# Kernel tuning notes

Hardware: AMD Instinct MI355X
Metric: run time of the kernel (lower is better)

The kernel has to match this reference:

```python
import jax, jax.numpy as jnp
import numpy as np

LEAK_RATE = 0.1
SPIKE_THRESHOLD = 0.5
MAX_DIM = 2560
R = 2048   # reservoir dim
D = 1024   # input dim
B = 4096   # batch


def setup_inputs() -> dict:
    key = jax.random.key(0)
    k1, k2, k3, k4, k5 = jax.random.split(key, 5)
    inputs = jax.random.normal(k1, (B, D), dtype=jnp.float32)
    prev_state = jax.random.normal(k2, (B, MAX_DIM), dtype=jnp.float32)
    W_in = jax.random.normal(k3, (R, D), dtype=jnp.float32) * (1.0 / np.sqrt(D))
    W_res = jax.random.normal(k4, (R, R), dtype=jnp.float32) * (1.0 / np.sqrt(R))
    W_gate = jax.random.normal(k5, (3 * R, D), dtype=jnp.float32) * (1.0 / np.sqrt(D))
    return {"inputs": inputs, "prev_state": prev_state,
            "W_in": W_in, "W_res": W_res, "W_gate": W_gate}


def reference(inputs, prev_state, W_in, W_res, W_gate):
    # Slice state to active reservoir width (W_res.shape[0] == R)
    prev = prev_state[:, :R]                                  # [B, R]
    input_part = jnp.matmul(inputs, W_in.T)                   # [B, R]
    reservoir_part = jnp.matmul(prev, W_res.T)                # [B, R]
    gate = jax.nn.sigmoid(jnp.matmul(inputs, W_gate.T))       # [B, 3R]
    i_gate, f_gate, o_gate = jnp.split(gate, 3, axis=-1)      # each [B, R]
    state = (1.0 - LEAK_RATE) * (f_gate * prev) \
        + LEAK_RATE * jnp.tanh(i_gate * (input_part + reservoir_part))
    state = o_gate * state
    # Spike threshold + soft reset
    state = jnp.where(state > SPIKE_THRESHOLD, state - SPIKE_THRESHOLD, state)
    # Pad up to max dynamic reservoir dim
    padded = jnp.pad(state, ((0, 0), (0, MAX_DIM - R)))       # [B, MAX_DIM]
    return padded
```

## Files before the change

kernel.cpp:

```cpp
#include <hip/hip_runtime.h>

#define B_  4096
#define D_  1024
#define R_  2048
#define MAXD 2560

typedef _Float16 half8 __attribute__((ext_vector_type(8)));
typedef _Float16 half4 __attribute__((ext_vector_type(4)));
typedef float    f32x4 __attribute__((ext_vector_type(4)));

constexpr int BM = 128;
constexpr int BN = 64;
constexpr int BK = 32;
constexpr int SAS = 40;

__device__ inline float sigmoidf_(float x) { return 1.0f / (1.0f + expf(-x)); }

__global__ __launch_bounds__(256, 2)
void reservoir_fused(const float* __restrict__ X,
                     const float* __restrict__ P,
                     const float* __restrict__ Win,
                     const float* __restrict__ Wres,
                     const float* __restrict__ Wg,
                     float* __restrict__ out)
{
    __shared__ _Float16 sAh[BM * SAS];
    __shared__ _Float16 sAl[BM * SAS];
    __shared__ _Float16 sWh[4][BN * SAS];
    __shared__ _Float16 sWl[4][BN * SAS];

    const int tid  = threadIdx.x;
    const int lane = tid & 63;
    const int wv   = tid >> 6;
    const int m0   = blockIdx.y * BM;
    const int n0   = blockIdx.x * BN;

    f32x4 acc[4][2][4];
    #pragma unroll
    for (int s = 0; s < 4; ++s)
        #pragma unroll
        for (int mt = 0; mt < 2; ++mt)
            #pragma unroll
            for (int nt = 0; nt < 4; ++nt) acc[s][mt][nt] = (f32x4){0.f, 0.f, 0.f, 0.f};

    const int fr = lane & 15;
    const int fk = (lane >> 4) * 8;

    for (int k0 = 0; k0 < D_ + R_; k0 += BK) {
        const bool ph1 = (k0 < D_);

        {
            const float* src; int ld, kc;
            if (ph1) { src = X; ld = D_;   kc = k0; }
            else     { src = P; ld = MAXD; kc = k0 - D_; }
            #pragma unroll
            for (int i = 0; i < 4; ++i) {
                int f = i * 256 + tid;
                int row = f >> 3, c4 = (f & 7) * 4;
                f32x4 v = *(const f32x4*)(src + (size_t)(m0 + row) * ld + kc + c4);
                half4 h, l;
                #pragma unroll
                for (int j = 0; j < 4; ++j) {
                    h[j] = (_Float16)v[j];
                    l[j] = (_Float16)(v[j] - (float)h[j]);
                }
                *(half4*)(&sAh[row * SAS + c4]) = h;
                *(half4*)(&sAl[row * SAS + c4]) = l;
            }
        }
        {
            const float* src; int ld, kc;
            if (ph1) { src = Win;  ld = D_; kc = k0; }
            else     { src = Wres; ld = R_; kc = k0 - D_; }
            #pragma unroll
            for (int i = 0; i < 2; ++i) {
                int f = i * 256 + tid;
                int row = f >> 3, c4 = (f & 7) * 4;
                f32x4 v = *(const f32x4*)(src + (size_t)(n0 + row) * ld + kc + c4);
                half4 h, l;
                #pragma unroll
                for (int j = 0; j < 4; ++j) {
                    h[j] = (_Float16)v[j];
                    l[j] = (_Float16)(v[j] - (float)h[j]);
                }
                *(half4*)(&sWh[0][row * SAS + c4]) = h;
                *(half4*)(&sWl[0][row * SAS + c4]) = l;
            }
        }
        if (ph1) {
            #pragma unroll
            for (int g = 0; g < 3; ++g)
                #pragma unroll
                for (int i = 0; i < 2; ++i) {
                    int f = i * 256 + tid;
                    int row = f >> 3, c4 = (f & 7) * 4;
                    f32x4 v = *(const f32x4*)(Wg + (size_t)(g * R_ + n0 + row) * D_ + k0 + c4);
                    half4 h, l;
                    #pragma unroll
                    for (int j = 0; j < 4; ++j) {
                        h[j] = (_Float16)v[j];
                        l[j] = (_Float16)(v[j] - (float)h[j]);
                    }
                    *(half4*)(&sWh[1 + g][row * SAS + c4]) = h;
                    *(half4*)(&sWl[1 + g][row * SAS + c4]) = l;
                }
        }
        __syncthreads();

        half8 ah0 = *(const half8*)(&sAh[(wv * 32 +      fr) * SAS + fk]);
        half8 al0 = *(const half8*)(&sAl[(wv * 32 +      fr) * SAS + fk]);
        half8 ah1 = *(const half8*)(&sAh[(wv * 32 + 16 + fr) * SAS + fk]);
        half8 al1 = *(const half8*)(&sAl[(wv * 32 + 16 + fr) * SAS + fk]);

        const int nsets = ph1 ? 4 : 1;
        #pragma unroll
        for (int s = 0; s < 4; ++s) {
            if (s < nsets) {
                #pragma unroll
                for (int nt = 0; nt < 4; ++nt) {
                    half8 bh = *(const half8*)(&sWh[s][(nt * 16 + fr) * SAS + fk]);
                    half8 bl = *(const half8*)(&sWl[s][(nt * 16 + fr) * SAS + fk]);
                    acc[s][0][nt] = __builtin_amdgcn_mfma_f32_16x16x32_f16(ah0, bh, acc[s][0][nt], 0, 0, 0);
                    acc[s][0][nt] = __builtin_amdgcn_mfma_f32_16x16x32_f16(al0, bh, acc[s][0][nt], 0, 0, 0);
                    acc[s][0][nt] = __builtin_amdgcn_mfma_f32_16x16x32_f16(ah0, bl, acc[s][0][nt], 0, 0, 0);
                    acc[s][1][nt] = __builtin_amdgcn_mfma_f32_16x16x32_f16(ah1, bh, acc[s][1][nt], 0, 0, 0);
                    acc[s][1][nt] = __builtin_amdgcn_mfma_f32_16x16x32_f16(al1, bh, acc[s][1][nt], 0, 0, 0);
                    acc[s][1][nt] = __builtin_amdgcn_mfma_f32_16x16x32_f16(ah1, bl, acc[s][1][nt], 0, 0, 0);
                }
            }
        }
        __syncthreads();
    }

    const int qd = lane >> 4;
    #pragma unroll
    for (int mt = 0; mt < 2; ++mt)
        #pragma unroll
        for (int nt = 0; nt < 4; ++nt)
            #pragma unroll
            for (int r = 0; r < 4; ++r) {
                int row = m0 + wv * 32 + mt * 16 + qd * 4 + r;
                int col = n0 + nt * 16 + fr;
                float pre = acc[0][mt][nt][r];
                float ig  = sigmoidf_(acc[1][mt][nt][r]);
                float fg  = sigmoidf_(acc[2][mt][nt][r]);
                float og  = sigmoidf_(acc[3][mt][nt][r]);
                float pv  = P[(size_t)row * MAXD + col];
                float st  = 0.9f * (fg * pv) + 0.1f * tanhf(ig * pre);
                st *= og;
                if (st > 0.5f) st -= 0.5f;
                out[(size_t)row * MAXD + col] = st;
            }
}

__global__ void pad_zero(float* __restrict__ out) {
    int idx = blockIdx.x * 256 + threadIdx.x;
    int row = idx >> 7;
    int c   = (idx & 127) * 4;
    *(f32x4*)(&out[(size_t)row * MAXD + R_ + c]) = (f32x4){0.f, 0.f, 0.f, 0.f};
}

extern "C" void kernel_launch(void* const* d_in, const int* in_sizes, int n_in,
                              void* d_out, int out_size, void* d_ws, size_t ws_size,
                              hipStream_t stream) {
    const float* X    = (const float*)d_in[0];
    const float* P    = (const float*)d_in[1];
    const float* Win  = (const float*)d_in[2];
    const float* Wres = (const float*)d_in[3];
    const float* Wg   = (const float*)d_in[4];
    float* out        = (float*)d_out;

    pad_zero<<<2048, 256, 0, stream>>>(out);
    dim3 grid(R_ / BN, B_ / BM);
    reservoir_fused<<<grid, 256, 0, stream>>>(X, P, Win, Wres, Wg, out);
}
```

Baseline: 526.0 us.

## Switch to 32x32x16 MFMA with 2x2 wave tiling and fragment-ordered LDS layout

Replaces the 16x16x32 MFMA tiles with 32x32x16 MFMA and reorganises the four waves into a 2x2 grid, each covering 64 rows by 32 columns. Shared memory is rewritten into a fragment-major layout so each lane reads its 8-half fragment contiguously, removing the padded row stride. The aim is fewer LDS reads per MFMA, no bank conflicts, and higher MFMA throughput per instruction. The epilogue index mapping changes to the 32x32 accumulator layout, which risks correctness errors if the mapping is wrong.

```diff
diff --git a/kernel.cpp b/kernel.cpp
--- a/kernel.cpp
+++ b/kernel.cpp
@@ -5,15 +5,23 @@
 #define R_  2048
 #define MAXD 2560
 
-typedef _Float16 half8 __attribute__((ext_vector_type(8)));
-typedef _Float16 half4 __attribute__((ext_vector_type(4)));
-typedef float    f32x4 __attribute__((ext_vector_type(4)));
+typedef _Float16 half4v __attribute__((ext_vector_type(4)));
+typedef _Float16 half8v __attribute__((ext_vector_type(8)));
+typedef float    f32x4  __attribute__((ext_vector_type(4)));
+typedef float    f32x16 __attribute__((ext_vector_type(16)));
 
 constexpr int BM = 128;
 constexpr int BN = 64;
 constexpr int BK = 32;
-constexpr int SAS = 40;
 
+
+__device__ inline void split4(const f32x4 v, half4v& h, half4v& l) {
+    #pragma unroll
+    for (int j = 0; j < 4; ++j) {
+        h[j] = (_Float16)v[j];
+        l[j] = (_Float16)(v[j] - (float)h[j]);
+    }
+}
 __device__ inline float sigmoidf_(float x) { return 1.0f / (1.0f + expf(-x)); }
 
 __global__ __launch_bounds__(256, 2)
@@ -24,27 +32,24 @@
                      const float* __restrict__ Wg,
                      float* __restrict__ out)
 {
-    __shared__ _Float16 sAh[BM * SAS];
-    __shared__ _Float16 sAl[BM * SAS];
-    __shared__ _Float16 sWh[4][BN * SAS];
-    __shared__ _Float16 sWl[4][BN * SAS];
+    __shared__ _Float16 sAh[4096], sAl[4096];
+    __shared__ _Float16 sWh[4][2048], sWl[4][2048];
 
     const int tid  = threadIdx.x;
     const int lane = tid & 63;
     const int wv   = tid >> 6;
+    const int wm   = wv >> 1;
+    const int wn   = wv & 1;
     const int m0   = blockIdx.y * BM;
     const int n0   = blockIdx.x * BN;
 
-    f32x4 acc[4][2][4];
+    f32x16 acc[4][2];
     #pragma unroll
     for (int s = 0; s < 4; ++s)
         #pragma unroll
-        for (int mt = 0; mt < 2; ++mt)
+        for (int mb = 0; mb < 2; ++mb)
             #pragma unroll
-            for (int nt = 0; nt < 4; ++nt) acc[s][mt][nt] = (f32x4){0.f, 0.f, 0.f, 0.f};
-
-    const int fr = lane & 15;
-    const int fk = (lane >> 4) * 8;
+            for (int r = 0; r < 16; ++r) acc[s][mb][r] = 0.0f;
 
     for (int k0 = 0; k0 < D_ + R_; k0 += BK) {
         const bool ph1 = (k0 < D_);
@@ -55,17 +60,13 @@
             else     { src = P; ld = MAXD; kc = k0 - D_; }
             #pragma unroll
             for (int i = 0; i < 4; ++i) {
-                int f = i * 256 + tid;
-                int row = f >> 3, c4 = (f & 7) * 4;
-                f32x4 v = *(const f32x4*)(src + (size_t)(m0 + row) * ld + kc + c4);
-                half4 h, l;
-                #pragma unroll
-                for (int j = 0; j < 4; ++j) {
-                    h[j] = (_Float16)v[j];
-                    l[j] = (_Float16)(v[j] - (float)h[j]);
-                }
-                *(half4*)(&sAh[row * SAS + c4]) = h;
-                *(half4*)(&sAl[row * SAS + c4]) = l;
+                int t = i * 256 + tid;
+                int r = t >> 3, sel = t & 7, kq = sel >> 1, h4 = sel & 1;
+                f32x4 v = *(const f32x4*)(src + (size_t)(m0 + r) * ld + kc + kq * 8 + h4 * 4);
+                half4v h, l; split4(v, h, l);
+                int off = ((r >> 5) * 2 + (kq >> 1)) * 512 + ((((kq & 1) << 5) | (r & 31)) * 8) + h4 * 4;
+                *(half4v*)(&sAh[off]) = h;
+                *(half4v*)(&sAl[off]) = l;
             }
         }
         {
@@ -74,17 +75,13 @@
             else     { src = Wres; ld = R_; kc = k0 - D_; }
             #pragma unroll
             for (int i = 0; i < 2; ++i) {
-                int f = i * 256 + tid;
-                int row = f >> 3, c4 = (f & 7) * 4;
-                f32x4 v = *(const f32x4*)(src + (size_t)(n0 + row) * ld + kc + c4);
-                half4 h, l;
-                #pragma unroll
-                for (int j = 0; j < 4; ++j) {
-                    h[j] = (_Float16)v[j];
-                    l[j] = (_Float16)(v[j] - (float)h[j]);
-                }
-                *(half4*)(&sWh[0][row * SAS + c4]) = h;
-                *(half4*)(&sWl[0][row * SAS + c4]) = l;
+                int t = i * 256 + tid;
+                int r = t >> 3, sel = t & 7, kq = sel >> 1, h4 = sel & 1;
+                f32x4 v = *(const f32x4*)(src + (size_t)(n0 + r) * ld + kc + kq * 8 + h4 * 4);
+                half4v h, l; split4(v, h, l);
+                int off = ((r >> 5) * 2 + (kq >> 1)) * 512 + ((((kq & 1) << 5) | (r & 31)) * 8) + h4 * 4;
+                *(half4v*)(&sWh[0][off]) = h;
+                *(half4v*)(&sWl[0][off]) = l;
             }
         }
         if (ph1) {
@@ -92,65 +89,56 @@
             for (int g = 0; g < 3; ++g)
                 #pragma unroll
                 for (int i = 0; i < 2; ++i) {
-                    int f = i * 256 + tid;
-                    int row = f >> 3, c4 = (f & 7) * 4;
-                    f32x4 v = *(const f32x4*)(Wg + (size_t)(g * R_ + n0 + row) * D_ + k0 + c4);
-                    half4 h, l;
-                    #pragma unroll
-                    for (int j = 0; j < 4; ++j) {
-                        h[j] = (_Float16)v[j];
-                        l[j] = (_Float16)(v[j] - (float)h[j]);
-                    }
-                    *(half4*)(&sWh[1 + g][row * SAS + c4]) = h;
-                    *(half4*)(&sWl[1 + g][row * SAS + c4]) = l;
+                    int t = i * 256 + tid;
+                    int r = t >> 3, sel = t & 7, kq = sel >> 1, h4 = sel & 1;
+                    f32x4 v = *(const f32x4*)(Wg + (size_t)(g * R_ + n0 + r) * D_ + k0 + kq * 8 + h4 * 4);
+                    half4v h, l; split4(v, h, l);
+                    int off = ((r >> 5) * 2 + (kq >> 1)) * 512 + ((((kq & 1) << 5) | (r & 31)) * 8) + h4 * 4;
+                    *(half4v*)(&sWh[1 + g][off]) = h;
+                    *(half4v*)(&sWl[1 + g][off]) = l;
                 }
         }
         __syncthreads();
 
-        half8 ah0 = *(const half8*)(&sAh[(wv * 32 +      fr) * SAS + fk]);
-        half8 al0 = *(const half8*)(&sAl[(wv * 32 +      fr) * SAS + fk]);
-        half8 ah1 = *(const half8*)(&sAh[(wv * 32 + 16 + fr) * SAS + fk]);
-        half8 al1 = *(const half8*)(&sAl[(wv * 32 + 16 + fr) * SAS + fk]);
-
-        const int nsets = ph1 ? 4 : 1;
         #pragma unroll
-        for (int s = 0; s < 4; ++s) {
-            if (s < nsets) {
-                #pragma unroll
-                for (int nt = 0; nt < 4; ++nt) {
-                    half8 bh = *(const half8*)(&sWh[s][(nt * 16 + fr) * SAS + fk]);
-                    half8 bl = *(const half8*)(&sWl[s][(nt * 16 + fr) * SAS + fk]);
-                    acc[s][0][nt] = __builtin_amdgcn_mfma_f32_16x16x32_f16(ah0, bh, acc[s][0][nt], 0, 0, 0);
-                    acc[s][0][nt] = __builtin_amdgcn_mfma_f32_16x16x32_f16(al0, bh, acc[s][0][nt], 0, 0, 0);
-                    acc[s][0][nt] = __builtin_amdgcn_mfma_f32_16x16x32_f16(ah0, bl, acc[s][0][nt], 0, 0, 0);
-                    acc[s][1][nt] = __builtin_amdgcn_mfma_f32_16x16x32_f16(ah1, bh, acc[s][1][nt], 0, 0, 0);
-                    acc[s][1][nt] = __builtin_amdgcn_mfma_f32_16x16x32_f16(al1, bh, acc[s][1][nt], 0, 0, 0);
-                    acc[s][1][nt] = __builtin_amdgcn_mfma_f32_16x16x32_f16(ah1, bl, acc[s][1][nt], 0, 0, 0);
-                }
+        for (int ks = 0; ks < 2; ++ks) {
+            half8v ah0 = *(const half8v*)(&sAh[((wm * 2 + 0) * 2 + ks) * 512 + lane * 8]);
+            half8v al0 = *(const half8v*)(&sAl[((wm * 2 + 0) * 2 + ks) * 512 + lane * 8]);
+            half8v ah1 = *(const half8v*)(&sAh[((wm * 2 + 1) * 2 + ks) * 512 + lane * 8]);
+            half8v al1 = *(const half8v*)(&sAl[((wm * 2 + 1) * 2 + ks) * 512 + lane * 8]);
+            #pragma unroll
+            for (int s = 0; s < 4; ++s) {
+                if (!ph1 && s > 0) continue;
+                half8v bh = *(const half8v*)(&sWh[s][(wn * 2 + ks) * 512 + lane * 8]);
+                half8v bl = *(const half8v*)(&sWl[s][(wn * 2 + ks) * 512 + lane * 8]);
+                acc[s][0] = __builtin_amdgcn_mfma_f32_32x32x16_f16(ah0, bh, acc[s][0], 0, 0, 0);
+                acc[s][0] = __builtin_amdgcn_mfma_f32_32x32x16_f16(al0, bh, acc[s][0], 0, 0, 0);
+                acc[s][0] = __builtin_amdgcn_mfma_f32_32x32x16_f16(ah0, bl, acc[s][0], 0, 0, 0);
+                acc[s][1] = __builtin_amdgcn_mfma_f32_32x32x16_f16(ah1, bh, acc[s][1], 0, 0, 0);
+                acc[s][1] = __builtin_amdgcn_mfma_f32_32x32x16_f16(al1, bh, acc[s][1], 0, 0, 0);
+                acc[s][1] = __builtin_amdgcn_mfma_f32_32x32x16_f16(ah1, bl, acc[s][1], 0, 0, 0);
             }
         }
         __syncthreads();
     }
 
-    const int qd = lane >> 4;
+    const int col = n0 + wn * 32 + (lane & 31);
+    const int rbase = m0 + wm * 64 + 4 * (lane >> 5);
     #pragma unroll
-    for (int mt = 0; mt < 2; ++mt)
+    for (int mb = 0; mb < 2; ++mb)
         #pragma unroll
-        for (int nt = 0; nt < 4; ++nt)
-            #pragma unroll
-            for (int r = 0; r < 4; ++r) {
-                int row = m0 + wv * 32 + mt * 16 + qd * 4 + r;
-                int col = n0 + nt * 16 + fr;
-                float pre = acc[0][mt][nt][r];
-                float ig  = sigmoidf_(acc[1][mt][nt][r]);
-                float fg  = sigmoidf_(acc[2][mt][nt][r]);
-                float og  = sigmoidf_(acc[3][mt][nt][r]);
-                float pv  = P[(size_t)row * MAXD + col];
-                float st  = 0.9f * (fg * pv) + 0.1f * tanhf(ig * pre);
-                st *= og;
-                if (st > 0.5f) st -= 0.5f;
-                out[(size_t)row * MAXD + col] = st;
-            }
+        for (int r = 0; r < 16; ++r) {
+            int row = rbase + mb * 32 + (r & 3) + 8 * (r >> 2);
+            float pre = acc[0][mb][r];
+            float ig  = sigmoidf_(acc[1][mb][r]);
+            float fg  = sigmoidf_(acc[2][mb][r]);
+            float og  = sigmoidf_(acc[3][mb][r]);
+            float pv  = P[(size_t)row * MAXD + col];
+            float st  = 0.9f * (fg * pv) + 0.1f * tanhf(ig * pre);
+            st *= og;
+            if (st > 0.5f) st -= 0.5f;
+            out[(size_t)row * MAXD + col] = st;
+        }
 }
 
 __global__ void pad_zero(float* __restrict__ out) {
```

After: 529.2 us. No clear change (+0.6%).
